# Performance work log

Hardware: AMD Instinct MI355X
Metric: run time of the kernel (lower is better)

## Reference

```python
import jax, jax.numpy as jnp
import numpy as np

# Model dims (match init_kwargs)
B, CIN, H, W = 4, 64, 32, 32
K, STRIDE, PAD = 3, 1, 1
OC, LMAX = 64, 144              # out channels, max taps per channel (pruned from 64*9=576)
HP, WP = H + 2 * PAD, W + 2 * PAD
HOUT = (H - K + 2 * PAD) // STRIDE + 1   # 32
WOUT = (W - K + 2 * PAD) // STRIDE + 1   # 32
P = HOUT * WOUT


def setup_inputs() -> dict:
    key = jax.random.key(0)
    ks = jax.random.split(key, 7)
    images = jax.random.normal(ks[0], (B, CIN, H, W), dtype=jnp.float32)
    # Taps: (in_channel, kh, kw) -> flat index into padded image, as in
    # image_weight_index = c*np_input_size + kh*col_size + kw
    c = jax.random.randint(ks[1], (OC, LMAX), 0, CIN)
    kh = jax.random.randint(ks[2], (OC, LMAX), 0, K)
    kw = jax.random.randint(ks[3], (OC, LMAX), 0, K)
    tap_idx = (c * (HP * WP) + kh * WP + kw).astype(jnp.int32)
    # Variable filter_length per output channel (CSR ragged), encoded here as a
    # zero-mask on padded taps -- mathematically identical to the CUDA loop bound.
    lengths = jax.random.randint(ks[4], (OC,), LMAX // 2, LMAX + 1)
    mask = (jnp.arange(LMAX)[None, :] < lengths[:, None]).astype(jnp.float32)
    tap_w = jax.random.normal(ks[5], (OC, LMAX), dtype=jnp.float32) * mask
    bias_index = jnp.arange(OC, dtype=jnp.int32)
    bias_value = jax.random.normal(ks[6], (OC,), dtype=jnp.float32)
    return {"images": images, "tap_idx": tap_idx, "tap_w": tap_w,
            "bias_index": bias_index, "bias_value": bias_value}


def reference(images, tap_idx, tap_w, bias_index, bias_value):
    # Zero-pad then flatten each batch image: [B, CIN*HP*WP]
    imgp = jnp.pad(images, ((0, 0), (0, 0), (PAD, PAD), (PAD, PAD)))
    flat = imgp.reshape(B, CIN * HP * WP)
    # Pixel offsets (image_range): h*stride*WP + w*stride, row-major -> [P]
    pix = (jnp.arange(HOUT)[:, None] * STRIDE * WP
           + jnp.arange(WOUT)[None, :] * STRIDE).reshape(-1)
    # Gather indices: [OC, LMAX, P]
    idx = tap_idx[:, :, None] + pix[None, None, :]
    gathered = flat[:, idx]                      # [B, OC, LMAX, P] irregular gather
    out = jnp.einsum('bolp,ol->bop', gathered, tap_w)   # [B, OC, P]
    # add_bias kernel: scatter bias_value into channels bias_index
    bias_full = jnp.zeros((OC,), dtype=jnp.float32).at[bias_index].add(bias_value)
    out = out + bias_full[None, :, None]
    # Original allocates output as [B, out_channels, W_out, H_out]
    return out.reshape(B, OC, WOUT, HOUT)
```

## Files before the change

kernel.cpp:

```cpp
#include <hip/hip_runtime.h>
#include <hip/hip_fp16.h>

#define B 4
#define CIN 64
#define OC 64
#define LMAX 144
#define HP 34
#define WP 34
#define HPW (HP*WP)
#define NPIX 1024
#define RSTR 34
#define NPR 18
#define CSTR (NPR*RSTR)
#define GUARD 4
#define TOT_H2 (GUARD + CIN*CSTR)

typedef _Float16 h2_t __attribute__((ext_vector_type(2)));
typedef unsigned long long u64;

static __device__ __forceinline__ unsigned pk(float lo, float hi) {
    return __builtin_bit_cast(unsigned, __builtin_amdgcn_cvt_pkrtz(lo, hi));
}

__global__ __launch_bounds__(512, 1) void reconv_r7(
    const float* __restrict__ images,
    const int* __restrict__ tap_idx, const float* __restrict__ tap_w,
    const int* __restrict__ bias_index, const float* __restrict__ bias_value,
    float* __restrict__ out)
{
    __shared__ unsigned int s_img[TOT_H2];

    const int bo = blockIdx.x;
    const int b = bo >> 6;
    const int o = bo & (OC - 1);
    const int t = threadIdx.x;
    const int lane = t & 63;

    const int* ti = tap_idx + o * LMAX;
    const float* tw = tap_w + o * LMAX;
    int vidx0 = ti[lane];
    int vidx1 = ti[64 + lane];
    int vidx2 = ti[128 + (lane & 15)];
    int vw0 = __float_as_int(tw[lane]);
    int vw1 = __float_as_int(tw[64 + lane]);
    int vw2 = __float_as_int(tw[128 + (lane & 15)]);

    float bv = (bias_index[lane] == o) ? bias_value[lane] : 0.f;
    bv += __shfl_xor(bv, 32); bv += __shfl_xor(bv, 16); bv += __shfl_xor(bv, 8);
    bv += __shfl_xor(bv, 4);  bv += __shfl_xor(bv, 2);  bv += __shfl_xor(bv, 1);
    const float bias = bv;

    const float4* img4 = (const float4*)images + (size_t)b * (CIN * 32 * 32 / 4);
    const int q = t & 7;
    const int g = t >> 3;
    #pragma unroll 4
    for (int i = 0; i < 16; ++i) {
        int rowid = i * 64 + g;
        int c = rowid >> 4;
        int ir = rowid & 15;
        float4 a = img4[c * 256 + ir * 8 + q];
        float4 d = img4[c * 256 + (ir + 16) * 8 + q];
        unsigned u0 = pk(a.x, d.x);
        unsigned u1 = pk(a.y, d.y);
        unsigned u2 = pk(a.z, d.z);
        unsigned u3 = pk(a.w, d.w);
        int e = GUARD + c * CSTR + (ir + 1) * RSTR + 4 * q;
        *(u64*)&s_img[e]     = ((u64)u1 << 32) | u0;
        *(u64*)&s_img[e + 2] = ((u64)u3 << 32) | u2;
    }
    for (int i = t; i < CIN * 8 * 2; i += 512) {
        int c = i >> 4;
        int r2 = i & 15;
        int which = r2 >> 3;
        int qq = r2 & 7;
        float4 v = img4[c * 256 + (which ? 16 : 15) * 8 + qq];
        unsigned u0 = which ? pk(v.x, 0.f) : pk(0.f, v.x);
        unsigned u1 = which ? pk(v.y, 0.f) : pk(0.f, v.y);
        unsigned u2 = which ? pk(v.z, 0.f) : pk(0.f, v.z);
        unsigned u3 = which ? pk(v.w, 0.f) : pk(0.f, v.w);
        int e = GUARD + c * CSTR + (which ? 17 : 0) * RSTR + 4 * qq;
        *(u64*)&s_img[e]     = ((u64)u1 << 32) | u0;
        *(u64*)&s_img[e + 2] = ((u64)u3 << 32) | u2;
    }

    int voff0, voff1, voff2;
    {
        int c0 = vidx0 / HPW, r0 = vidx0 - c0 * HPW, kh0 = r0 / WP, kw0 = r0 - kh0 * WP;
        voff0 = (GUARD + c0 * CSTR + kh0 * RSTR + kw0 - 1) * 4;
        int c1 = vidx1 / HPW, r1 = vidx1 - c1 * HPW, kh1 = r1 / WP, kw1 = r1 - kh1 * WP;
        voff1 = (GUARD + c1 * CSTR + kh1 * RSTR + kw1 - 1) * 4;
        int c2 = vidx2 / HPW, r2 = vidx2 - c2 * HPW, kh2 = r2 / WP, kw2 = r2 - kh2 * WP;
        voff2 = (GUARD + c2 * CSTR + kh2 * RSTR + kw2 - 1) * 4;
    }

    u64* s64 = (u64*)s_img;
    if (t == 0) { s64[0] = 0ull; s64[1] = 0ull; }
    for (int i = t; i < CIN * NPR; i += 512) {
        int c = i / NPR;
        int pr = i - c * NPR;
        int e = GUARD + c * CSTR + pr * RSTR + 32;
        *(u64*)&s_img[e] = 0ull;
    }

    __syncthreads();

    const int w = t & 31;
    const int h0 = t >> 5;
    const int pxb = (h0 * RSTR + w) * 4;
    const char* sbase = (const char*)s_img;
    float a0 = 0.f, a1 = 0.f;
    #pragma unroll
    for (int j = 0; j < LMAX; ++j) {
        int vo, vw;
        if (j < 64)       { vo = __builtin_amdgcn_readlane(voff0, j);
                            vw = __builtin_amdgcn_readlane(vw0, j); }
        else if (j < 128) { vo = __builtin_amdgcn_readlane(voff1, j - 64);
                            vw = __builtin_amdgcn_readlane(vw1, j - 64); }
        else              { vo = __builtin_amdgcn_readlane(voff2, j - 128);
                            vw = __builtin_amdgcn_readlane(vw2, j - 128); }
        __half2 hv = *(const __half2*)(sbase + (vo + pxb));
        float wgt = __int_as_float(vw);
        a0 = fmaf(wgt, __low2float(hv), a0);
        a1 = fmaf(wgt, __high2float(hv), a1);
    }

    float* op = out + (size_t)bo * NPIX;
    op[h0 * 32 + w] = a0 + bias;
    op[(h0 + 16) * 32 + w] = a1 + bias;
}

extern "C" void kernel_launch(void* const* d_in, const int* in_sizes, int n_in,
                              void* d_out, int out_size, void* d_ws, size_t ws_size,
                              hipStream_t stream) {
    const float* images     = (const float*)d_in[0];
    const int*   tap_idx    = (const int*)d_in[1];
    const float* tap_w      = (const float*)d_in[2];
    const int*   bias_index = (const int*)d_in[3];
    const float* bias_value = (const float*)d_in[4];
    float* out = (float*)d_out;

    reconv_r7<<<B * OC, 512, 0, stream>>>(images, tap_idx, tap_w,
                                          bias_index, bias_value, out);
}
```

Baseline: 12.51 us.

## Preformat padded fp16 image in workspace, stream into LDS via direct global-to-LDS loads

Adds a separate kernel that converts each batch image into the packed half2, padded row layout once and writes it to the workspace. The main conv kernel then copies that prebuilt layout straight into shared memory with global_load_lds DMA instead of having each of the 64 blocks per batch redo the fp32 load, conversion and padding writes. This removes repeated conversion work and register traffic. In exchange it adds a second kernel launch and a round trip through global memory.

```diff
diff --git a/kernel.cpp b/kernel.cpp
--- a/kernel.cpp
+++ b/kernel.cpp
@@ -14,27 +14,72 @@
 #define CSTR (NPR*RSTR)
 #define GUARD 4
 #define TOT_H2 (GUARD + CIN*CSTR)
+#define NCHUNK (TOT_H2/4)
 
-typedef _Float16 h2_t __attribute__((ext_vector_type(2)));
 typedef unsigned long long u64;
+typedef __attribute__((address_space(1))) const unsigned glb_u32;
+typedef __attribute__((address_space(3))) unsigned lds_u32;
 
 static __device__ __forceinline__ unsigned pk(float lo, float hi) {
     return __builtin_bit_cast(unsigned, __builtin_amdgcn_cvt_pkrtz(lo, hi));
 }
 
-__global__ __launch_bounds__(512, 1) void reconv_r7(
-    const float* __restrict__ images,
+__global__ __launch_bounds__(256) void format_kernel(
+    const float* __restrict__ images, unsigned* __restrict__ ws) {
+    __shared__ float ch[1024];
+    const int bc = blockIdx.x;
+    const int b = bc >> 6;
+    const int c = bc & 63;
+    const int t = threadIdx.x;
+    const float* src = images + (size_t)bc * 1024;
+    #pragma unroll
+    for (int i = 0; i < 4; ++i) ch[i * 256 + t] = src[i * 256 + t];
+    __syncthreads();
+    unsigned* dst = ws + (size_t)b * TOT_H2 + GUARD + c * CSTR;
+    for (int s = t; s < CSTR; s += 256) {
+        int pr = s / RSTR;
+        int cc = s - pr * RSTR;
+        float lo = 0.f, hi = 0.f;
+        int rlo = pr - 1;
+        int rhi = pr + 15;
+        if (cc < 32) {
+            if ((unsigned)rlo < 32u) lo = ch[rlo * 32 + cc];
+            if ((unsigned)rhi < 32u) hi = ch[rhi * 32 + cc];
+        }
+        dst[s] = pk(lo, hi);
+    }
+    if (c == 0 && t < GUARD) ws[(size_t)b * TOT_H2 + t] = 0u;
+}
+
+__global__ __launch_bounds__(512, 1) void reconv_r8(
+    const unsigned* __restrict__ wsimg,
     const int* __restrict__ tap_idx, const float* __restrict__ tap_w,
     const int* __restrict__ bias_index, const float* __restrict__ bias_value,
     float* __restrict__ out)
 {
-    __shared__ unsigned int s_img[TOT_H2];
+    __shared__ unsigned s_img[TOT_H2];
 
     const int bo = blockIdx.x;
     const int b = bo >> 6;
     const int o = bo & (OC - 1);
     const int t = threadIdx.x;
     const int lane = t & 63;
+    const int wid = t >> 6;
+
+    const unsigned* src = wsimg + (size_t)b * TOT_H2;
+    #pragma unroll
+    for (int r = 0; r < 19; ++r) {
+        int chunk = r * 512 + t;
+        glb_u32* gp = (glb_u32*)(src + chunk * 4);
+        lds_u32* lp = (lds_u32*)(s_img + (r * 512 + wid * 64) * 4);
+        __builtin_amdgcn_global_load_lds(gp, lp, 16, 0, 0);
+    }
+    if (t < 65) {
+        int chunk = 19 * 512 + t;
+        glb_u32* gp = (glb_u32*)(src + chunk * 4);
+        lds_u32* lp = (lds_u32*)(s_img + (19 * 512 + wid * 64) * 4);
+        __builtin_amdgcn_global_load_lds(gp, lp, 16, 0, 0);
+    }
 
     const int* ti = tap_idx + o * LMAX;
     const float* tw = tap_w + o * LMAX;
@@ -50,39 +95,6 @@
     bv += __shfl_xor(bv, 4);  bv += __shfl_xor(bv, 2);  bv += __shfl_xor(bv, 1);
     const float bias = bv;
 
-    const float4* img4 = (const float4*)images + (size_t)b * (CIN * 32 * 32 / 4);
-    const int q = t & 7;
-    const int g = t >> 3;
-    #pragma unroll 4
-    for (int i = 0; i < 16; ++i) {
-        int rowid = i * 64 + g;
-        int c = rowid >> 4;
-        int ir = rowid & 15;
-        float4 a = img4[c * 256 + ir * 8 + q];
-        float4 d = img4[c * 256 + (ir + 16) * 8 + q];
-        unsigned u0 = pk(a.x, d.x);
-        unsigned u1 = pk(a.y, d.y);
-        unsigned u2 = pk(a.z, d.z);
-        unsigned u3 = pk(a.w, d.w);
-        int e = GUARD + c * CSTR + (ir + 1) * RSTR + 4 * q;
-        *(u64*)&s_img[e]     = ((u64)u1 << 32) | u0;
-        *(u64*)&s_img[e + 2] = ((u64)u3 << 32) | u2;
-    }
-    for (int i = t; i < CIN * 8 * 2; i += 512) {
-        int c = i >> 4;
-        int r2 = i & 15;
-        int which = r2 >> 3;
-        int qq = r2 & 7;
-        float4 v = img4[c * 256 + (which ? 16 : 15) * 8 + qq];
-        unsigned u0 = which ? pk(v.x, 0.f) : pk(0.f, v.x);
-        unsigned u1 = which ? pk(v.y, 0.f) : pk(0.f, v.y);
-        unsigned u2 = which ? pk(v.z, 0.f) : pk(0.f, v.z);
-        unsigned u3 = which ? pk(v.w, 0.f) : pk(0.f, v.w);
-        int e = GUARD + c * CSTR + (which ? 17 : 0) * RSTR + 4 * qq;
-        *(u64*)&s_img[e]     = ((u64)u1 << 32) | u0;
-        *(u64*)&s_img[e + 2] = ((u64)u3 << 32) | u2;
-    }
-
     int voff0, voff1, voff2;
     {
         int c0 = vidx0 / HPW, r0 = vidx0 - c0 * HPW, kh0 = r0 / WP, kw0 = r0 - kh0 * WP;
@@ -91,15 +103,6 @@
         voff1 = (GUARD + c1 * CSTR + kh1 * RSTR + kw1 - 1) * 4;
         int c2 = vidx2 / HPW, r2 = vidx2 - c2 * HPW, kh2 = r2 / WP, kw2 = r2 - kh2 * WP;
         voff2 = (GUARD + c2 * CSTR + kh2 * RSTR + kw2 - 1) * 4;
-    }
-
-    u64* s64 = (u64*)s_img;
-    if (t == 0) { s64[0] = 0ull; s64[1] = 0ull; }
-    for (int i = t; i < CIN * NPR; i += 512) {
-        int c = i / NPR;
-        int pr = i - c * NPR;
-        int e = GUARD + c * CSTR + pr * RSTR + 32;
-        *(u64*)&s_img[e] = 0ull;
     }
 
     __syncthreads();
@@ -138,7 +141,9 @@
     const int*   bias_index = (const int*)d_in[3];
     const float* bias_value = (const float*)d_in[4];
     float* out = (float*)d_out;
+    unsigned* wsimg = (unsigned*)d_ws;
 
-    reconv_r7<<<B * OC, 512, 0, stream>>>(images, tap_idx, tap_w,
+    format_kernel<<<B * CIN, 256, 0, stream>>>(images, wsimg);
+    reconv_r8<<<B * OC, 512, 0, stream>>>(wsimg, tap_idx, tap_w,
                                           bias_index, bias_value, out);
 }
```

Result: slower. 16.75 us (+34.0%).
